# Performance work log

Hardware: AMD Instinct MI355X
Metric: run time of the kernel (lower is better)

The kernel has to match this reference:

```python
import jax, jax.numpy as jnp
import numpy as np

N_VARS = 1024      # code length n
N_CHECKS = 512     # number of parity checks m
VAR_DEG = 3        # column degree -> E = N_VARS * VAR_DEG edges
N_EDGES = N_VARS * VAR_DEG
BATCH = 2048
CLIP_TANH = 10.0
ENSEMBLE_NUM = 3


def _make_edges():
    # Regular LDPC-like Tanner graph: each variable node connects to VAR_DEG distinct checks.
    rng = np.random.default_rng(0)
    edge_var = np.repeat(np.arange(N_VARS, dtype=np.int32), VAR_DEG)
    edge_chk = np.concatenate([
        rng.choice(N_CHECKS, size=VAR_DEG, replace=False).astype(np.int32)
        for _ in range(N_VARS)
    ])
    return jnp.asarray(edge_var), jnp.asarray(edge_chk)


def setup_inputs() -> dict:
    key = jax.random.key(0)
    k1, k2, k3, k4, k5 = jax.random.split(key, 5)
    edge_var, edge_chk = _make_edges()
    return {
        "x": jax.random.normal(k1, (BATCH, N_EDGES), dtype=jnp.float32),
        "llr": jax.random.normal(k2, (BATCH, N_VARS), dtype=jnp.float32),
        "odd_weights": jax.random.normal(k3, (N_EDGES, N_EDGES), dtype=jnp.float32) * 0.05,
        "llr_weights": jax.random.normal(k4, (N_VARS, N_EDGES), dtype=jnp.float32) * 0.05,
        "dropout_logits": jnp.full((N_EDGES,), 3.0, dtype=jnp.float32),  # LOGITS_INIT
        "edge_var": edge_var,
        "edge_chk": edge_chk,
    }


def reference(x, llr, odd_weights, llr_weights, dropout_logits, edge_var, edge_chk):
    dt = x.dtype
    # Tanner-graph masks (constant connectivity)
    # w_skipconn2even_mask: [n, E], 1 where edge e is incident to variable v
    w_skip_mask = (jnp.arange(N_VARS)[:, None] == edge_var[None, :]).astype(dt)
    # w_odd2even_mask: [E, E], 1 where edges share a variable but differ in check (extrinsic)
    w_odd_mask = ((edge_var[:, None] == edge_var[None, :]) &
                  (edge_chk[:, None] != edge_chk[None, :])).astype(dt)

    x_after_mask = x @ (w_odd_mask * odd_weights)                 # [B, E]
    odd_weights_times_llr = llr @ (w_skip_mask * llr_weights)     # [B, E]

    keep_prob = jax.nn.sigmoid(dropout_logits)                    # [E]
    keys = jax.random.split(jax.random.key(42), ENSEMBLE_NUM)

    def member(k):
        u = jax.random.uniform(k, odd_weights_times_llr.shape, dtype=dt)
        z = (u < keep_prob).astype(dt)                            # dropout_ori
        odd = jnp.clip(x_after_mask + odd_weights_times_llr * z,
                       -CLIP_TANH, CLIP_TANH)
        return jnp.tanh(0.5 * odd)

    return jnp.mean(jax.vmap(member)(keys), axis=0)              # ensemble average
```

## Files before the change

kernel.cpp:

```cpp
#include <hip/hip_runtime.h>
#include <stdint.h>
#include <cmath>

#define NVARS   1024
#define NEDGES  3072
#define BATCHSZ 2048
#define RPT     4
#define ROWSTR  (BATCHSZ/RPT)
#define LOG2E   1.4426950408889634f

__host__ __device__ __forceinline__ uint32_t rotl32(uint32_t x, int r) {
#if defined(__HIP_DEVICE_COMPILE__)
    return __builtin_amdgcn_alignbit(x, x, (uint32_t)(32 - r));
#else
    return (x << r) | (x >> (32 - r));
#endif
}

__host__ __forceinline__ void threefry2x32_host(uint32_t k0, uint32_t k1,
                                                uint32_t x0, uint32_t x1,
                                                uint32_t& o0, uint32_t& o1) {
    uint32_t k2 = k0 ^ k1 ^ 0x1BD11BDAu;
    const int rots[20] = {13,15,26,6, 17,29,16,24, 13,15,26,6, 17,29,16,24, 13,15,26,6};
    x0 += k0; x1 += k1;
    int rc = 0;
    const uint32_t ka[5] = {k1, k2, k0, k1, k2};
    const uint32_t kb[5] = {k2, k0, k1, k2, k0};
    for (int g = 0; g < 5; g++) {
        for (int i = 0; i < 4; i++) {
            x0 += x1; x1 = rotl32(x1, rots[rc++]); x1 ^= x0;
        }
        x0 += ka[g]; x1 += kb[g] + (uint32_t)(g + 1);
    }
    o0 = x0; o1 = x1;
}

__device__ __forceinline__ void threefry_quad_xor(
        uint32_t k0, uint32_t k1,
        uint32_t i0, uint32_t i1, uint32_t i2, uint32_t i3,
        uint32_t& m0, uint32_t& m1, uint32_t& m2, uint32_t& m3) {
    uint32_t k2 = k0 ^ k1 ^ 0x1BD11BDAu;
    uint32_t a0 = k0, a1 = i0 + k1;
    uint32_t b0 = k0, b1 = i1 + k1;
    uint32_t c0 = k0, c1 = i2 + k1;
    uint32_t d0 = k0, d1 = i3 + k1;
#define ROT4(r) \
    a1 = rotl32(a1, r); b1 = rotl32(b1, r); c1 = rotl32(c1, r); d1 = rotl32(d1, r); \
    a1 ^= a0; b1 ^= b0; c1 ^= c0; d1 ^= d0;
#define R4(r) \
    a0 += a1; b0 += b1; c0 += c1; d0 += d1; \
    ROT4(r)
#define IR4(ka, kb, r) \
    a1 += (kb); b1 += (kb); c1 += (kb); d1 += (kb); \
    a0 = a0 + (ka) + a1; b0 = b0 + (ka) + b1; \
    c0 = c0 + (ka) + c1; d0 = d0 + (ka) + d1; \
    ROT4(r)
    R4(13) R4(15) R4(26) R4(6)
    IR4(k1, k2 + 1u, 17) R4(29) R4(16) R4(24)
    IR4(k2, k0 + 2u, 13) R4(15) R4(26) R4(6)
    IR4(k0, k1 + 3u, 17) R4(29) R4(16) R4(24)
    IR4(k1, k2 + 4u, 13) R4(15) R4(26) R4(6)
#undef R4
#undef IR4
#undef ROT4
    m0 = (a0 + k2) ^ (a1 + k0 + 5u);
    m1 = (b0 + k2) ^ (b1 + k0 + 5u);
    m2 = (c0 + k2) ^ (c1 + k0 + 5u);
    m3 = (d0 + k2) ^ (d1 + k0 + 5u);
}

__device__ __forceinline__ float tanh_half_2(float o2) {
    float ex = __builtin_amdgcn_exp2f(o2);
    return 1.0f - 2.0f * __builtin_amdgcn_rcpf(ex + 1.0f);
}

__global__ void setup_kernel(const float* __restrict__ oddw,
                             const float* __restrict__ llrw,
                             const float* __restrict__ logits,
                             const int* __restrict__ evar,
                             const int* __restrict__ echk,
                             float4* __restrict__ wkp,
                             int4* __restrict__ sidx) {
    int e = blockIdx.x * blockDim.x + threadIdx.x;
    if (e >= NEDGES) return;
    int v = evar[e];
    int r = e % 3;
    int base = e - r;
    int o1 = base + ((r + 1) % 3);
    int o2 = base + ((r + 2) % 3);
    int ce = echk[e];
    float w1 = (echk[o1] != ce) ? oddw[(size_t)o1 * NEDGES + e] * LOG2E : 0.0f;
    float w2 = (echk[o2] != ce) ? oddw[(size_t)o2 * NEDGES + e] * LOG2E : 0.0f;
    float vw = llrw[(size_t)v * NEDGES + e] * LOG2E;
    float kpf = (float)(1.0 / (1.0 + exp(-(double)logits[e])));
    double Td = ceil((double)kpf * 8388608.0);
    uint32_t T9;
    if (Td >= 8388608.0) T9 = 0xFFFFFFFFu;
    else                 T9 = ((uint32_t)Td) << 9;
    wkp[e]  = make_float4(w1, w2, vw, __uint_as_float(T9));
    sidx[e] = make_int4(o1, o2, v, 0);
}

#define ISTEP ((uint32_t)ROWSTR * NEDGES)
#define XSTEP (ISTEP * 4u)
#define LSTEP ((uint32_t)ROWSTR * NVARS * 4u)

__global__ __launch_bounds__(256, 8) void
odd_layer_kernel(const float* __restrict__ x, const float* __restrict__ llr,
                 const float4* __restrict__ wkp, const int4* __restrict__ sidx,
                 float* __restrict__ out,
                 uint32_t k0a, uint32_t k1a, uint32_t k0b, uint32_t k1b,
                 uint32_t k0c, uint32_t k1c) {
    const int e  = blockIdx.x * 256 + threadIdx.x;
    const int b0 = blockIdx.y;

    const char* xb = (const char*)(x   + (size_t)b0 * NEDGES);
    const char* lb = (const char*)(llr + (size_t)b0 * NVARS);
    char*       ob = (char*)      (out + (size_t)b0 * NEDGES);

    float4 w = wkp[e];
    int4   s = sidx[e];
    const uint32_t T9 = __float_as_uint(w.w);

    const uint32_t i0 = (uint32_t)b0 * NEDGES + (uint32_t)e;
    const uint32_t i1 = i0 + ISTEP, i2 = i0 + 2u * ISTEP, i3 = i0 + 3u * ISTEP;

    uint32_t p0, p1, p2, p3;
    threefry_quad_xor(k0a, k1a, i0, i1, i2, i3, p0, p1, p2, p3);

    const uint32_t sx4 = (uint32_t)s.x << 2;
    const uint32_t sy4 = (uint32_t)s.y << 2;
    const uint32_t sz4 = (uint32_t)s.z << 2;
    float xv1[RPT], xv2[RPT], lvv[RPT];
#pragma unroll
    for (int r = 0; r < RPT; r++) {
        xv1[r] = *(const float*)(xb + (sx4 + r * XSTEP));
        xv2[r] = *(const float*)(xb + (sy4 + r * XSTEP));
        lvv[r] = *(const float*)(lb + (sz4 + r * LSTEP));
    }
    __builtin_amdgcn_sched_barrier(0);

    uint32_t q0, q1, q2, q3, r0, r1, r2, r3;
    threefry_quad_xor(k0b, k1b, i0, i1, i2, i3, q0, q1, q2, q3);
    threefry_quad_xor(k0c, k1c, i0, i1, i2, i3, r0, r1, r2, r3);

    int cnt[RPT];
    cnt[0] = ((p0 < T9) ? 1 : 0) + ((q0 < T9) ? 1 : 0) + ((r0 < T9) ? 1 : 0);
    cnt[1] = ((p1 < T9) ? 1 : 0) + ((q1 < T9) ? 1 : 0) + ((r1 < T9) ? 1 : 0);
    cnt[2] = ((p2 < T9) ? 1 : 0) + ((q2 < T9) ? 1 : 0) + ((r2 < T9) ? 1 : 0);
    cnt[3] = ((p3 < T9) ? 1 : 0) + ((q3 < T9) ? 1 : 0) + ((r3 < T9) ? 1 : 0);

    const uint32_t e4 = (uint32_t)e << 2;
#pragma unroll
    for (int r = 0; r < RPT; r++) {
        float xa = fmaf(xv2[r], w.y, xv1[r] * w.x);
        float t0 = tanh_half_2(xa);
        float t1 = tanh_half_2(fmaf(lvv[r], w.z, xa));
        float cf = (float)cnt[r];
        float res = fmaf(cf, (t1 - t0) * (1.0f / 3.0f), t0);
        __builtin_nontemporal_store(res, (float*)(ob + (e4 + r * XSTEP)));
    }
}

extern "C" void kernel_launch(void* const* d_in, const int* in_sizes, int n_in,
                              void* d_out, int out_size, void* d_ws, size_t ws_size,
                              hipStream_t stream) {
    const float* x      = (const float*)d_in[0];
    const float* llr    = (const float*)d_in[1];
    const float* oddw   = (const float*)d_in[2];
    const float* llrw   = (const float*)d_in[3];
    const float* logits = (const float*)d_in[4];
    const int*   evar   = (const int*)d_in[5];
    const int*   echk   = (const int*)d_in[6];
    float* out = (float*)d_out;

    float4* wkp  = (float4*)d_ws;
    int4*   sidx = (int4*)((char*)d_ws + (size_t)NEDGES * sizeof(float4));

    uint32_t k0[3], k1[3];
    for (uint32_t j = 0; j < 3; j++) {
        threefry2x32_host(0u, 42u, 0u, j, k0[j], k1[j]);
    }

    setup_kernel<<<48, 64, 0, stream>>>(oddw, llrw, logits, evar, echk, wkp, sidx);

    dim3 grid(NEDGES / 256, ROWSTR);
    odd_layer_kernel<<<grid, 256, 0, stream>>>(x, llr, wkp, sidx, out,
                                               k0[0], k1[0], k0[1], k1[1], k0[2], k1[2]);
}
```

Before: 44.05 us.

## Fuse setup into main kernel and process eight rows per thread

Removes the separate setup kernel launch. Each thread of the main kernel now gathers its own odd/llr weights, check indices and logit, and computes the keep threshold inline, including a double-precision sigmoid. Rows per thread go from 4 to 8, which halves the grid and spreads that per-edge setup over more batch rows. It also assumes edge_var = e/3 rather than reading it, and drops the sched_barrier. The costs are extra scattered weight loads per block, double-precision math in every thread, higher register pressure from 24 RNG words, and fewer blocks for latency hiding.

```diff
diff --git a/kernel.cpp b/kernel.cpp
--- a/kernel.cpp
+++ b/kernel.cpp
@@ -5,7 +5,7 @@
 #define NVARS   1024
 #define NEDGES  3072
 #define BATCHSZ 2048
-#define RPT     4
+#define RPT     8
 #define ROWSTR  (BATCHSZ/RPT)
 #define LOG2E   1.4426950408889634f
 
@@ -74,63 +74,41 @@
     return 1.0f - 2.0f * __builtin_amdgcn_rcpf(ex + 1.0f);
 }
 
-__global__ void setup_kernel(const float* __restrict__ oddw,
-                             const float* __restrict__ llrw,
-                             const float* __restrict__ logits,
-                             const int* __restrict__ evar,
-                             const int* __restrict__ echk,
-                             float4* __restrict__ wkp,
-                             int4* __restrict__ sidx) {
-    int e = blockIdx.x * blockDim.x + threadIdx.x;
-    if (e >= NEDGES) return;
-    int v = evar[e];
-    int r = e % 3;
-    int base = e - r;
-    int o1 = base + ((r + 1) % 3);
-    int o2 = base + ((r + 2) % 3);
-    int ce = echk[e];
-    float w1 = (echk[o1] != ce) ? oddw[(size_t)o1 * NEDGES + e] * LOG2E : 0.0f;
-    float w2 = (echk[o2] != ce) ? oddw[(size_t)o2 * NEDGES + e] * LOG2E : 0.0f;
-    float vw = llrw[(size_t)v * NEDGES + e] * LOG2E;
-    float kpf = (float)(1.0 / (1.0 + exp(-(double)logits[e])));
-    double Td = ceil((double)kpf * 8388608.0);
-    uint32_t T9;
-    if (Td >= 8388608.0) T9 = 0xFFFFFFFFu;
-    else                 T9 = ((uint32_t)Td) << 9;
-    wkp[e]  = make_float4(w1, w2, vw, __uint_as_float(T9));
-    sidx[e] = make_int4(o1, o2, v, 0);
-}
-
 #define ISTEP ((uint32_t)ROWSTR * NEDGES)
 #define XSTEP (ISTEP * 4u)
 #define LSTEP ((uint32_t)ROWSTR * NVARS * 4u)
 
 __global__ __launch_bounds__(256, 8) void
-odd_layer_kernel(const float* __restrict__ x, const float* __restrict__ llr,
-                 const float4* __restrict__ wkp, const int4* __restrict__ sidx,
-                 float* __restrict__ out,
-                 uint32_t k0a, uint32_t k1a, uint32_t k0b, uint32_t k1b,
-                 uint32_t k0c, uint32_t k1c) {
+odd_layer_fused(const float* __restrict__ x, const float* __restrict__ llr,
+                const float* __restrict__ oddw, const float* __restrict__ llrw,
+                const float* __restrict__ logits, const int* __restrict__ echk,
+                float* __restrict__ out,
+                uint32_t k0a, uint32_t k1a, uint32_t k0b, uint32_t k1b,
+                uint32_t k0c, uint32_t k1c) {
     const int e  = blockIdx.x * 256 + threadIdx.x;
     const int b0 = blockIdx.y;
+
+    const int v    = e / 3;
+    const int r3   = e - v * 3;
+    const int base = v * 3;
+    const int o1 = base + ((r3 + 1) == 3 ? 0 : r3 + 1);
+    const int o2 = base + (r3 == 0 ? 2 : r3 - 1);
+
+    const float w1r = oddw[(size_t)o1 * NEDGES + e];
+    const float w2r = oddw[(size_t)o2 * NEDGES + e];
+    const float vwr = llrw[(size_t)v * NEDGES + e];
+    const float lg  = logits[e];
+    const int   ce  = echk[e];
+    const int   c1  = echk[o1];
+    const int   c2  = echk[o2];
 
     const char* xb = (const char*)(x   + (size_t)b0 * NEDGES);
     const char* lb = (const char*)(llr + (size_t)b0 * NVARS);
     char*       ob = (char*)      (out + (size_t)b0 * NEDGES);
 
-    float4 w = wkp[e];
-    int4   s = sidx[e];
-    const uint32_t T9 = __float_as_uint(w.w);
-
-    const uint32_t i0 = (uint32_t)b0 * NEDGES + (uint32_t)e;
-    const uint32_t i1 = i0 + ISTEP, i2 = i0 + 2u * ISTEP, i3 = i0 + 3u * ISTEP;
-
-    uint32_t p0, p1, p2, p3;
-    threefry_quad_xor(k0a, k1a, i0, i1, i2, i3, p0, p1, p2, p3);
-
-    const uint32_t sx4 = (uint32_t)s.x << 2;
-    const uint32_t sy4 = (uint32_t)s.y << 2;
-    const uint32_t sz4 = (uint32_t)s.z << 2;
+    const uint32_t sx4 = (uint32_t)o1 << 2;
+    const uint32_t sy4 = (uint32_t)o2 << 2;
+    const uint32_t sz4 = (uint32_t)v << 2;
     float xv1[RPT], xv2[RPT], lvv[RPT];
 #pragma unroll
     for (int r = 0; r < RPT; r++) {
@@ -138,26 +116,38 @@
         xv2[r] = *(const float*)(xb + (sy4 + r * XSTEP));
         lvv[r] = *(const float*)(lb + (sz4 + r * LSTEP));
     }
-    __builtin_amdgcn_sched_barrier(0);
 
-    uint32_t q0, q1, q2, q3, r0, r1, r2, r3;
-    threefry_quad_xor(k0b, k1b, i0, i1, i2, i3, q0, q1, q2, q3);
-    threefry_quad_xor(k0c, k1c, i0, i1, i2, i3, r0, r1, r2, r3);
+    const uint32_t i0 = (uint32_t)b0 * NEDGES + (uint32_t)e;
 
-    int cnt[RPT];
-    cnt[0] = ((p0 < T9) ? 1 : 0) + ((q0 < T9) ? 1 : 0) + ((r0 < T9) ? 1 : 0);
-    cnt[1] = ((p1 < T9) ? 1 : 0) + ((q1 < T9) ? 1 : 0) + ((r1 < T9) ? 1 : 0);
-    cnt[2] = ((p2 < T9) ? 1 : 0) + ((q2 < T9) ? 1 : 0) + ((r2 < T9) ? 1 : 0);
-    cnt[3] = ((p3 < T9) ? 1 : 0) + ((q3 < T9) ? 1 : 0) + ((r3 < T9) ? 1 : 0);
+    uint32_t m[3][RPT];
+#pragma unroll
+    for (int j = 0; j < 3; j++) {
+        const uint32_t kk0 = (j == 0) ? k0a : (j == 1) ? k0b : k0c;
+        const uint32_t kk1 = (j == 0) ? k1a : (j == 1) ? k1b : k1c;
+        threefry_quad_xor(kk0, kk1, i0,              i0 + ISTEP,
+                                     i0 + 2u * ISTEP, i0 + 3u * ISTEP,
+                          m[j][0], m[j][1], m[j][2], m[j][3]);
+        threefry_quad_xor(kk0, kk1, i0 + 4u * ISTEP, i0 + 5u * ISTEP,
+                                     i0 + 6u * ISTEP, i0 + 7u * ISTEP,
+                          m[j][4], m[j][5], m[j][6], m[j][7]);
+    }
+
+    const float kpf = (float)(1.0 / (1.0 + exp(-(double)lg)));
+    const double Td = ceil((double)kpf * 8388608.0);
+    const uint32_t T9 = (Td >= 8388608.0) ? 0xFFFFFFFFu : (((uint32_t)Td) << 9);
+    const float w1 = (c1 != ce) ? w1r * LOG2E : 0.0f;
+    const float w2 = (c2 != ce) ? w2r * LOG2E : 0.0f;
+    const float vw = vwr * LOG2E;
 
     const uint32_t e4 = (uint32_t)e << 2;
 #pragma unroll
     for (int r = 0; r < RPT; r++) {
-        float xa = fmaf(xv2[r], w.y, xv1[r] * w.x);
+        const int cnt = ((m[0][r] < T9) ? 1 : 0) + ((m[1][r] < T9) ? 1 : 0)
+                      + ((m[2][r] < T9) ? 1 : 0);
+        float xa = fmaf(xv2[r], w2, xv1[r] * w1);
         float t0 = tanh_half_2(xa);
-        float t1 = tanh_half_2(fmaf(lvv[r], w.z, xa));
-        float cf = (float)cnt[r];
-        float res = fmaf(cf, (t1 - t0) * (1.0f / 3.0f), t0);
+        float t1 = tanh_half_2(fmaf(lvv[r], vw, xa));
+        float res = fmaf((float)cnt, (t1 - t0) * (1.0f / 3.0f), t0);
         __builtin_nontemporal_store(res, (float*)(ob + (e4 + r * XSTEP)));
     }
 }
@@ -170,21 +160,17 @@
     const float* oddw   = (const float*)d_in[2];
     const float* llrw   = (const float*)d_in[3];
     const float* logits = (const float*)d_in[4];
-    const int*   evar   = (const int*)d_in[5];
     const int*   echk   = (const int*)d_in[6];
     float* out = (float*)d_out;
-
-    float4* wkp  = (float4*)d_ws;
-    int4*   sidx = (int4*)((char*)d_ws + (size_t)NEDGES * sizeof(float4));
 
     uint32_t k0[3], k1[3];
     for (uint32_t j = 0; j < 3; j++) {
         threefry2x32_host(0u, 42u, 0u, j, k0[j], k1[j]);
     }
 
-    setup_kernel<<<48, 64, 0, stream>>>(oddw, llrw, logits, evar, echk, wkp, sidx);
-
     dim3 grid(NEDGES / 256, ROWSTR);
-    odd_layer_kernel<<<grid, 256, 0, stream>>>(x, llr, wkp, sidx, out,
-                                               k0[0], k1[0], k0[1], k1[1], k0[2], k1[2]);
+    odd_layer_fused<<<grid, 256, 0, stream>>>(x, llr, oddw, llrw, logits, echk,
+                                              out,
+                                              k0[0], k1[0], k0[1], k1[1],
+                                              k0[2], k1[2]);
 }
```

Measured after the change: 42.48 us (median of 2 runs). -3.6%, faster.
